# Optimization experiments

Measured on AMD Instinct MI355X. Metric: run time of the kernel, lower is better.

## Reference

```python
import jax, jax.numpy as jnp
import numpy as np

F = 256   # nb_features
H = 8     # nb_heads
B = 4
S = 1024  # q_s == kv_s
SCALE = F ** 0.5  # module MULTIPLIES scores by sqrt(f) when scale=True


def setup_inputs() -> dict:
    key = jax.random.key(0)
    ks = jax.random.split(key, 6)
    return {
        "q_input": jax.random.normal(ks[0], (B, F, S), dtype=jnp.float32),
        "kv_input": jax.random.normal(ks[1], (B, F, S), dtype=jnp.float32),
        "Wq": jax.random.normal(ks[2], (F, F * H), dtype=jnp.float32) * (F ** -0.5),
        "Wk": jax.random.normal(ks[3], (F, F * H), dtype=jnp.float32) * (F ** -0.5),
        "Wv": jax.random.normal(ks[4], (F, F * H), dtype=jnp.float32) * (F ** -0.5),
        "Wz": jax.random.normal(ks[5], (F * H, F), dtype=jnp.float32) * ((F * H) ** -0.5),
    }


def reference(q_input, kv_input, Wq, Wk, Wv, Wz):
    b, f, q_s = q_input.shape
    kv_s = kv_input.shape[2]
    h = H
    # (b, f, s) -> (b, s, f)
    qx = jnp.transpose(q_input, (0, 2, 1))
    kvx = jnp.transpose(kv_input, (0, 2, 1))
    # Linear f -> f*h, then split last dim into (f, h)
    q = (qx @ Wq).reshape(b, q_s, f, h)
    k = (kvx @ Wk).reshape(b, kv_s, f, h)
    v = (kvx @ Wv).reshape(b, kv_s, f, h)
    # sigmoid-gated attention: scores MULTIPLIED by sqrt(f)
    qkt = jnp.einsum('bifh,bjfh->bijh', q, k)
    attn = jax.nn.sigmoid(qkt * SCALE)
    weighted_v = jnp.einsum('bijh,bjfh->bifh', attn, v)  # (b, q_s, f, h)
    z = weighted_v.reshape(b * q_s, f * h)
    out = jax.nn.relu(z @ Wz)  # dropout p=0.0 -> identity
    return jnp.transpose(out.reshape(b, q_s, f), (0, 2, 1))  # (b, f, q_s)
```

## Files before the change

kernel.cpp:

```cpp
#include <hip/hip_runtime.h>
#include <hip/hip_fp16.h>

typedef _Float16 f16;
typedef _Float16 f16x8 __attribute__((ext_vector_type(8)));
typedef float f32x4 __attribute__((ext_vector_type(4)));

#define AS1(p) ((const __attribute__((address_space(1))) void*)(p))
#define AS3(p) ((__attribute__((address_space(3))) void*)(p))

__device__ __forceinline__ void gload16(const void* g, void* l) {
  __builtin_amdgcn_global_load_lds(AS1(g), AS3(l), 16, 0, 0);
}

__device__ __forceinline__ float sgm(float x) {
  return __builtin_amdgcn_rcpf(1.0f + __builtin_amdgcn_exp2f(x * -23.083120654223414f));
}

__device__ __forceinline__ unsigned pack2(float a, float b) {
  union { f16 h[2]; unsigned u; } x;
  x.h[0] = (f16)a; x.h[1] = (f16)b;
  return x.u;
}

__device__ __forceinline__ void tbody(const float* __restrict__ ip,
                                      f16* __restrict__ op,
                                      long in_rs, long out_rs) {
  __shared__ float t[64][68];
  int tid = threadIdx.x;
  {
    int c4 = (tid & 15) * 4, r0 = tid >> 4;
#pragma unroll
    for (int p = 0; p < 4; ++p) {
      int r = r0 + 16 * p;
      float4 v = *(const float4*)(ip + (long)r * in_rs + c4);
      t[c4 + 0][r] = v.x; t[c4 + 1][r] = v.y; t[c4 + 2][r] = v.z; t[c4 + 3][r] = v.w;
    }
  }
  __syncthreads();
  {
    int r4 = (tid & 15) * 4, c0 = tid >> 4;
#pragma unroll
    for (int p = 0; p < 4; ++p) {
      int c = c0 + 16 * p;
      float4 v = *(const float4*)(&t[c][r4]);
      union { f16 h[4]; unsigned long long u; } pk;
      pk.h[0] = (f16)v.x; pk.h[1] = (f16)v.y; pk.h[2] = (f16)v.z; pk.h[3] = (f16)v.w;
      *(unsigned long long*)(op + (long)c * out_rs + r4) = pk.u;
    }
  }
}

__global__ __launch_bounds__(256) void tin(const float* __restrict__ qin,
                                           const float* __restrict__ kvin,
                                           f16* __restrict__ Xq, f16* __restrict__ Xkv) {
  int z = blockIdx.z;
  const float* in = (z < 4) ? qin : kvin;
  f16* out = (z < 4) ? Xq : Xkv;
  long b = z & 3;
  tbody(in + b * 262144 + (long)(blockIdx.y * 64) * 1024 + blockIdx.x * 64,
        out + b * 262144 + (long)(blockIdx.x * 64) * 256 + blockIdx.y * 64,
        1024, 256);
}

__global__ __launch_bounds__(256) void tw3(const float* __restrict__ Wq,
                                           const float* __restrict__ Wk,
                                           const float* __restrict__ Wv,
                                           f16* __restrict__ Wqt, f16* __restrict__ Wkt,
                                           f16* __restrict__ Wvt) {
  int z = blockIdx.z;
  const float* in = (z == 0) ? Wq : (z == 1) ? Wk : Wv;
  f16* out = (z == 0) ? Wqt : (z == 1) ? Wkt : Wvt;
  tbody(in + (long)(blockIdx.y * 64) * 2048 + blockIdx.x * 64,
        out + (long)(blockIdx.x * 64) * 256 + blockIdx.y * 64,
        2048, 256);
}

__global__ __launch_bounds__(256) void twz(const float* __restrict__ Wz,
                                           f16* __restrict__ Wzt) {
  long z = blockIdx.z;
  tbody(Wz + z * 256 + (long)(blockIdx.y * 64) * 2048 + blockIdx.x * 64,
        Wzt + z * 256 + (long)(blockIdx.x * 64) * 2048 + blockIdx.y * 64,
        2048, 2048);
}

__global__ __launch_bounds__(256) void projk(
    const f16* __restrict__ Xq, const f16* __restrict__ Xkv,
    const f16* __restrict__ Wqt, const f16* __restrict__ Wkt, const f16* __restrict__ Wvt,
    f16* __restrict__ Qh, f16* __restrict__ Kh, f16* __restrict__ Vt) {
  __shared__ char sm[65536];
  int z = blockIdx.z;
  const f16* A = (z == 0) ? Xq : Xkv;
  const f16* B = (z == 0) ? Wqt : (z == 1) ? Wkt : Wvt;
  int m0 = blockIdx.x * 128, n0 = blockIdx.y * 128;
  int tid = threadIdx.x, wave = tid >> 6, lane = tid & 63;
  int wm = wave & 1, wn = wave >> 1;
  f32x4 acc[4][4];
#pragma unroll
  for (int i = 0; i < 4; ++i)
#pragma unroll
    for (int j = 0; j < 4; ++j) acc[i][j] = (f32x4){0.f, 0.f, 0.f, 0.f};

  auto PSTAGE = [&](int buf, int kt) {
    char* As = sm + buf * 32768;
    char* Bs = As + 16384;
    int k0 = kt * 64;
#pragma unroll
    for (int is = 0; is < 4; ++is) {
      int loff = is * 4096 + wave * 1024;
      int g = loff + lane * 16;
      int row = g >> 7, sl = (g >> 4) & 7;
      int sp = (sl ^ (row & 7)) * 8;
      gload16(A + (long)(m0 + row) * 256 + k0 + sp, As + loff);
      gload16(B + (long)(n0 + row) * 256 + k0 + sp, Bs + loff);
    }
  };

  PSTAGE(0, 0);
  __syncthreads();
  for (int kt = 0; kt < 4; ++kt) {
    int cur = kt & 1;
    if (kt < 3) PSTAGE(cur ^ 1, kt + 1);
    const char* As = sm + cur * 32768;
    const char* Bs = As + 16384;
#pragma unroll
    for (int t = 0; t < 2; ++t) {
      f16x8 af[4], bf[4];
#pragma unroll
      for (int mi = 0; mi < 4; ++mi) {
        int row = wm * 64 + mi * 16 + (lane & 15);
        int sl = (t * 4 + (lane >> 4)) ^ (row & 7);
        af[mi] = *(const f16x8*)(As + row * 128 + sl * 16);
      }
#pragma unroll
      for (int ni = 0; ni < 4; ++ni) {
        int row = wn * 64 + ni * 16 + (lane & 15);
        int sl = (t * 4 + (lane >> 4)) ^ (row & 7);
        bf[ni] = *(const f16x8*)(Bs + row * 128 + sl * 16);
      }
#pragma unroll
      for (int mi = 0; mi < 4; ++mi)
#pragma unroll
        for (int ni = 0; ni < 4; ++ni)
          acc[mi][ni] = __builtin_amdgcn_mfma_f32_16x16x32_f16(af[mi], bf[ni], acc[mi][ni], 0, 0, 0);
    }
    __syncthreads();
  }
#pragma unroll
  for (int mi = 0; mi < 4; ++mi)
#pragma unroll
    for (int ni = 0; ni < 4; ++ni) {
      int cc = wn * 64 + ni * 16 + (lane & 15);
      int rs0 = wm * 64 + mi * 16 + (lane >> 4) * 4;
      union { f16 h[4]; unsigned long long u; } pk;
#pragma unroll
      for (int r = 0; r < 4; ++r) pk.h[r] = (f16)acc[mi][ni][r];
      *(unsigned long long*)(sm + cc * 272 + rs0 * 2) = pk.u;
    }
  __syncthreads();
  if (z < 2) {
    f16* outp = (z == 0) ? Qh : Kh;
#pragma unroll
    for (int pass = 0; pass < 4; ++pass) {
      int item = pass * 256 + tid;
      int rs = item & 127, h = item >> 7;
      int m = m0 + rs, b = m >> 10, s = m & 1023;
      union { unsigned short u16[16]; uint4 q[2]; } pk;
#pragma unroll
      for (int u = 0; u < 16; ++u)
        pk.u16[u] = *(const unsigned short*)(sm + (h + 8 * u) * 272 + rs * 2);
      f16* dst = outp + ((long)(b * 8 + h) * 1024 + s) * 256 + (n0 >> 3);
      *(uint4*)dst = pk.q[0];
      *(uint4*)(dst + 8) = pk.q[1];
    }
  } else {
    int cc = tid >> 1, half = tid & 1;
    int c = n0 + cc, h = c & 7, fi = c >> 3;
    int m = m0 + half * 64;
    int b = m >> 10, s0 = m & 1023;
    uint4 q[8];
#pragma unroll
    for (int j = 0; j < 8; ++j)
      q[j] = *(const uint4*)(sm + cc * 272 + half * 128 + j * 16);
    f16* dst = Vt + ((long)(b * 8 + h) * 256 + fi) * 1024 + s0;
#pragma unroll
    for (int j = 0; j < 8; ++j) *(uint4*)(dst + j * 8) = q[j];
  }
}

__global__ __launch_bounds__(256) void attnk(
    const f16* __restrict__ Qh, const f16* __restrict__ Kh,
    const f16* __restrict__ Vt, f16* __restrict__ Zb) {
  __shared__ char sm[65536];
  int flat = blockIdx.x;
  int xcd = flat & 7, slotb = flat >> 3;
  int bh = xcd + 8 * (slotb & 3);
  int i0 = (slotb >> 2) * 64;
  int tid = threadIdx.x, wave = tid >> 6, lane = tid & 63;
  int l15 = lane & 15, l4 = lane >> 4;
  const f16* Qp = Qh + (long)bh * 262144;
  const f16* Kp = Kh + (long)bh * 262144;
  const f16* Vp = Vt + (long)bh * 262144;
  f16x8 q[8];
  {
    const f16* qr = Qp + (long)(i0 + wave * 16 + l15) * 256 + l4 * 8;
#pragma unroll
    for (int t = 0; t < 8; ++t) q[t] = *(const f16x8*)(qr + t * 32);
  }
  f32x4 acc[16];
#pragma unroll
  for (int n = 0; n < 16; ++n) acc[n] = (f32x4){0.f, 0.f, 0.f, 0.f};

  auto STAGE = [&](int buf, int j0) {
    char* Ks = sm + buf * 32768;
    char* Vs = Ks + 16384;
#pragma unroll
    for (int is = 0; is < 4; ++is) {
      int loff = is * 4096 + wave * 1024;
      int g = loff + lane * 16;
      {
        int row = g >> 9, sl = (g >> 4) & 31;
        gload16(Kp + (long)(j0 + row) * 256 + ((sl ^ row) * 8), Ks + loff);
      }
      {
        int f = g >> 6, jc = (g >> 4) & 3;
        gload16(Vp + (long)f * 1024 + j0 + jc * 8, Vs + loff);
      }
    }
  };

  STAGE(0, 0);
  __syncthreads();
  for (int jt = 0; jt < 32; ++jt) {
    int cur = jt & 1;
    if (jt < 31) STAGE(cur ^ 1, (jt + 1) * 32);
    const char* Ks = sm + cur * 32768;
    const char* Vs = Ks + 16384;
    f32x4 s0 = (f32x4){0.f, 0.f, 0.f, 0.f};
    f32x4 s1 = (f32x4){0.f, 0.f, 0.f, 0.f};
#pragma unroll
    for (int t = 0; t < 8; ++t) {
      int c = t * 4 + l4;
      f16x8 k0 = *(const f16x8*)(Ks + l15 * 512 + ((c ^ l15) * 16));
      f16x8 k1 = *(const f16x8*)(Ks + (16 + l15) * 512 + ((c ^ (16 + l15)) * 16));
      s0 = __builtin_amdgcn_mfma_f32_16x16x32_f16(k0, q[t], s0, 0, 0, 0);
      s1 = __builtin_amdgcn_mfma_f32_16x16x32_f16(k1, q[t], s1, 0, 0, 0);
    }
    unsigned u00 = pack2(sgm(s0[0]), sgm(s0[1]));
    unsigned u01 = pack2(sgm(s0[2]), sgm(s0[3]));
    unsigned u10 = pack2(sgm(s1[0]), sgm(s1[1]));
    unsigned u11 = pack2(sgm(s1[2]), sgm(s1[3]));
    auto a0 = __builtin_amdgcn_permlane32_swap(u00, u10, false, false);
    auto w02 = __builtin_amdgcn_permlane16_swap(a0[0], a0[1], false, false);
    auto a1 = __builtin_amdgcn_permlane32_swap(u01, u11, false, false);
    auto w13 = __builtin_amdgcn_permlane16_swap(a1[0], a1[1], false, false);
    union { unsigned u[4]; f16x8 v; } pa;
    pa.u[0] = w02[0]; pa.u[1] = w13[0]; pa.u[2] = w02[1]; pa.u[3] = w13[1];
#pragma unroll
    for (int n = 0; n < 16; ++n) {
      f16x8 vb = *(const f16x8*)(Vs + (n * 16 + l15) * 64 + l4 * 16);
      acc[n] = __builtin_amdgcn_mfma_f32_16x16x32_f16(pa.v, vb, acc[n], 0, 0, 0);
    }
    __syncthreads();
  }
#pragma unroll
  for (int nf = 0; nf < 16; ++nf)
#pragma unroll
    for (int r = 0; r < 4; ++r) {
      int il = wave * 16 + l4 * 4 + r;
      int f = nf * 16 + l15;
      *(f16*)(sm + il * 512 + ((f * 2) ^ (((il >> 2) & 3) << 5))) = (f16)acc[nf][r];
    }
  __syncthreads();
  f16* zp = Zb + ((long)bh * 1024 + i0) * 256;
#pragma unroll
  for (int c = 0; c < 8; ++c) {
    int il = c * 8 + (tid >> 5);
    int fb = (tid & 31) * 16;
    uint4 v = *(const uint4*)(sm + il * 512 + (fb ^ (((il >> 2) & 3) << 5)));
    *(uint4*)((char*)zp + il * 512 + fb) = v;
  }
}

__global__ __launch_bounds__(256) void zkern(
    const f16* __restrict__ Wzt, const f16* __restrict__ Zb,
    float* __restrict__ out) {
  __shared__ char sm[32768];
  int fo0 = blockIdx.x * 64, s0 = blockIdx.y * 64, b = blockIdx.z;
  int tid = threadIdx.x, wave = tid >> 6, lane = tid & 63;
  int wm = wave & 1, wn = wave >> 1;
  f32x4 acc[2][2];
#pragma unroll
  for (int i = 0; i < 2; ++i)
#pragma unroll
    for (int j = 0; j < 2; ++j) acc[i][j] = (f32x4){0.f, 0.f, 0.f, 0.f};

  auto ZSTAGE = [&](int buf, int kt) {
    char* As = sm + buf * 16384;
    char* Bs = As + 8192;
    int k0 = kt * 64, h = k0 >> 8, fi0 = k0 & 255;
#pragma unroll
    for (int is = 0; is < 2; ++is) {
      int loff = is * 4096 + wave * 1024;
      int g = loff + lane * 16;
      int row = g >> 7, sl = (g >> 4) & 7;
      int sp = (sl ^ (row & 7)) * 8;
      gload16(Wzt + (long)(fo0 + row) * 2048 + k0 + sp, As + loff);
      gload16(Zb + ((long)(b * 8 + h) * 1024 + s0 + row) * 256 + fi0 + sp, Bs + loff);
    }
  };

  ZSTAGE(0, 0);
  __syncthreads();
  for (int kt = 0; kt < 32; ++kt) {
    int cur = kt & 1;
    if (kt < 31) ZSTAGE(cur ^ 1, kt + 1);
    const char* As = sm + cur * 16384;
    const char* Bs = As + 8192;
#pragma unroll
    for (int t = 0; t < 2; ++t) {
      f16x8 af[2], bf[2];
#pragma unroll
      for (int mi = 0; mi < 2; ++mi) {
        int row = wm * 32 + mi * 16 + (lane & 15);
        int sl = (t * 4 + (lane >> 4)) ^ (row & 7);
        af[mi] = *(const f16x8*)(As + row * 128 + sl * 16);
      }
#pragma unroll
      for (int ni = 0; ni < 2; ++ni) {
        int row = wn * 32 + ni * 16 + (lane & 15);
        int sl = (t * 4 + (lane >> 4)) ^ (row & 7);
        bf[ni] = *(const f16x8*)(Bs + row * 128 + sl * 16);
      }
#pragma unroll
      for (int mi = 0; mi < 2; ++mi)
#pragma unroll
        for (int ni = 0; ni < 2; ++ni)
          acc[mi][ni] = __builtin_amdgcn_mfma_f32_16x16x32_f16(af[mi], bf[ni], acc[mi][ni], 0, 0, 0);
    }
    __syncthreads();
  }
#pragma unroll
  for (int mi = 0; mi < 2; ++mi)
#pragma unroll
    for (int ni = 0; ni < 2; ++ni)
#pragma unroll
      for (int r = 0; r < 4; ++r) {
        int fo = fo0 + wm * 32 + mi * 16 + (lane >> 4) * 4 + r;
        int s = s0 + wn * 32 + ni * 16 + (lane & 15);
        float v = acc[mi][ni][r];
        out[((long)b * 256 + fo) * 1024 + s] = v > 0.f ? v : 0.f;
      }
}

extern "C" void kernel_launch(void* const* d_in, const int* in_sizes, int n_in,
                              void* d_out, int out_size, void* d_ws, size_t ws_size,
                              hipStream_t stream) {
  const float* qin = (const float*)d_in[0];
  const float* kvin = (const float*)d_in[1];
  const float* Wq = (const float*)d_in[2];
  const float* Wk = (const float*)d_in[3];
  const float* Wv = (const float*)d_in[4];
  const float* Wz = (const float*)d_in[5];
  float* out = (float*)d_out;
  char* ws = (char*)d_ws;
  const long MB = 1 << 20;
  f16* Xq  = (f16*)(ws + 0 * MB);
  f16* Xkv = (f16*)(ws + 2 * MB);
  f16* Wqt = (f16*)(ws + 4 * MB);
  f16* Wkt = (f16*)(ws + 5 * MB);
  f16* Wvt = (f16*)(ws + 6 * MB);
  f16* Wzt = (f16*)(ws + 7 * MB);
  f16* Qh  = (f16*)(ws + 8 * MB);
  f16* Kh  = (f16*)(ws + 24 * MB);
  f16* Vt  = (f16*)(ws + 40 * MB);
  f16* Zb  = Qh;
  dim3 blk(256);
  tin<<<dim3(16, 4, 8), blk, 0, stream>>>(qin, kvin, Xq, Xkv);
  tw3<<<dim3(32, 4, 3), blk, 0, stream>>>(Wq, Wk, Wv, Wqt, Wkt, Wvt);
  twz<<<dim3(4, 4, 8), blk, 0, stream>>>(Wz, Wzt);
  projk<<<dim3(32, 16, 3), blk, 0, stream>>>(Xq, Xkv, Wqt, Wkt, Wvt, Qh, Kh, Vt);
  attnk<<<dim3(512), blk, 0, stream>>>(Qh, Kh, Vt, Zb);
  zkern<<<dim3(4, 16, 4), blk, 0, stream>>>(Wzt, Zb, out);
}
```

Measured before the change: 128.1 us.

## Merge transpose kernels and streamline attention loop addressing and scheduling

The three input and weight transpose kernels are merged into one launch over a flat grid of 1024 blocks, removing two kernel launches. In the attention kernel, global K/V pointers are precomputed and advanced each tile instead of recomputing addresses. The V tile in LDS gets an XOR swizzle to reduce bank conflicts, and buffer selection is done by XOR on offsets. The loop also adds s_setprio around the MFMA sections and uses cvt_pkrtz for the fp16 packing, which rounds toward zero instead of to nearest.

Result: faster. 118.2 us (-7.7%).

```diff
diff --git a/kernel.cpp b/kernel.cpp
--- a/kernel.cpp
+++ b/kernel.cpp
@@ -3,7 +3,9 @@
 
 typedef _Float16 f16;
 typedef _Float16 f16x8 __attribute__((ext_vector_type(8)));
+typedef _Float16 h16x2 __attribute__((ext_vector_type(2)));
 typedef float f32x4 __attribute__((ext_vector_type(4)));
+typedef unsigned u32x4 __attribute__((ext_vector_type(4)));
 
 #define AS1(p) ((const __attribute__((address_space(1))) void*)(p))
 #define AS3(p) ((__attribute__((address_space(3))) void*)(p))
@@ -14,12 +16,6 @@
 
 __device__ __forceinline__ float sgm(float x) {
   return __builtin_amdgcn_rcpf(1.0f + __builtin_amdgcn_exp2f(x * -23.083120654223414f));
-}
-
-__device__ __forceinline__ unsigned pack2(float a, float b) {
-  union { f16 h[2]; unsigned u; } x;
-  x.h[0] = (f16)a; x.h[1] = (f16)b;
-  return x.u;
 }
 
 __device__ __forceinline__ void tbody(const float* __restrict__ ip,
@@ -50,37 +46,35 @@
   }
 }
 
-__global__ __launch_bounds__(256) void tin(const float* __restrict__ qin,
-                                           const float* __restrict__ kvin,
-                                           f16* __restrict__ Xq, f16* __restrict__ Xkv) {
-  int z = blockIdx.z;
-  const float* in = (z < 4) ? qin : kvin;
-  f16* out = (z < 4) ? Xq : Xkv;
-  long b = z & 3;
-  tbody(in + b * 262144 + (long)(blockIdx.y * 64) * 1024 + blockIdx.x * 64,
-        out + b * 262144 + (long)(blockIdx.x * 64) * 256 + blockIdx.y * 64,
-        1024, 256);
-}
-
-__global__ __launch_bounds__(256) void tw3(const float* __restrict__ Wq,
-                                           const float* __restrict__ Wk,
-                                           const float* __restrict__ Wv,
-                                           f16* __restrict__ Wqt, f16* __restrict__ Wkt,
-                                           f16* __restrict__ Wvt) {
-  int z = blockIdx.z;
-  const float* in = (z == 0) ? Wq : (z == 1) ? Wk : Wv;
-  f16* out = (z == 0) ? Wqt : (z == 1) ? Wkt : Wvt;
-  tbody(in + (long)(blockIdx.y * 64) * 2048 + blockIdx.x * 64,
-        out + (long)(blockIdx.x * 64) * 256 + blockIdx.y * 64,
-        2048, 256);
-}
-
-__global__ __launch_bounds__(256) void twz(const float* __restrict__ Wz,
-                                           f16* __restrict__ Wzt) {
-  long z = blockIdx.z;
-  tbody(Wz + z * 256 + (long)(blockIdx.y * 64) * 2048 + blockIdx.x * 64,
-        Wzt + z * 256 + (long)(blockIdx.x * 64) * 2048 + blockIdx.y * 64,
-        2048, 2048);
+__global__ __launch_bounds__(256) void tall(
+    const float* __restrict__ qin, const float* __restrict__ kvin,
+    const float* __restrict__ Wq, const float* __restrict__ Wk,
+    const float* __restrict__ Wv, const float* __restrict__ Wz,
+    f16* __restrict__ Xq, f16* __restrict__ Xkv,
+    f16* __restrict__ Wqt, f16* __restrict__ Wkt, f16* __restrict__ Wvt,
+    f16* __restrict__ Wzt) {
+  int id = blockIdx.x;
+  if (id < 512) {
+    int x = id & 15, y = (id >> 4) & 3, z = id >> 6;
+    const float* in = (z < 4) ? qin : kvin;
+    f16* out = (z < 4) ? Xq : Xkv;
+    long b = z & 3;
+    tbody(in + b * 262144 + (long)(y * 64) * 1024 + x * 64,
+          out + b * 262144 + (long)(x * 64) * 256 + y * 64, 1024, 256);
+  } else if (id < 896) {
+    int t = id - 512;
+    int x = t & 31, y = (t >> 5) & 3, z = t >> 7;
+    const float* in = (z == 0) ? Wq : (z == 1) ? Wk : Wv;
+    f16* out = (z == 0) ? Wqt : (z == 1) ? Wkt : Wvt;
+    tbody(in + (long)(y * 64) * 2048 + x * 64,
+          out + (long)(x * 64) * 256 + y * 64, 2048, 256);
+  } else {
+    int t = id - 896;
+    int x = t & 3, y = (t >> 2) & 3;
+    long z = t >> 4;
+    tbody(Wz + z * 256 + (long)(y * 64) * 2048 + x * 64,
+          Wzt + z * 256 + (long)(x * 64) * 2048 + y * 64, 2048, 2048);
+  }
 }
 
 __global__ __launch_bounds__(256) void projk(
@@ -198,8 +192,6 @@
   int tid = threadIdx.x, wave = tid >> 6, lane = tid & 63;
   int l15 = lane & 15, l4 = lane >> 4;
   const f16* Qp = Qh + (long)bh * 262144;
-  const f16* Kp = Kh + (long)bh * 262144;
-  const f16* Vp = Vt + (long)bh * 262144;
   f16x8 q[8];
   {
     const f16* qr = Qp + (long)(i0 + wave * 16 + l15) * 256 + l4 * 8;
@@ -210,57 +202,72 @@
 #pragma unroll
   for (int n = 0; n < 16; ++n) acc[n] = (f32x4){0.f, 0.f, 0.f, 0.f};
 
-  auto STAGE = [&](int buf, int j0) {
-    char* Ks = sm + buf * 32768;
-    char* Vs = Ks + 16384;
+  const char* kp[4];
+  const char* vp[4];
+  {
+    const char* Kb = (const char*)(Kh + (long)bh * 262144);
+    const char* Vb = (const char*)(Vt + (long)bh * 262144);
 #pragma unroll
     for (int is = 0; is < 4; ++is) {
-      int loff = is * 4096 + wave * 1024;
-      int g = loff + lane * 16;
-      {
-        int row = g >> 9, sl = (g >> 4) & 31;
-        gload16(Kp + (long)(j0 + row) * 256 + ((sl ^ row) * 8), Ks + loff);
-      }
-      {
-        int f = g >> 6, jc = (g >> 4) & 3;
-        gload16(Vp + (long)f * 1024 + j0 + jc * 8, Vs + loff);
-      }
+      int g = is * 4096 + wave * 1024 + lane * 16;
+      int krow = g >> 9, ksl = (g >> 4) & 31;
+      kp[is] = Kb + krow * 512 + ((ksl ^ krow) * 16);
+      int f = g >> 6, jc = (g >> 4) & 3;
+      vp[is] = Vb + f * 2048 + ((jc ^ ((f >> 1) & 3)) * 16);
+    }
+  }
+  const int KB  = l15 * 512 + ((l4 * 16) ^ (l15 * 16));
+  const int KB2 = KB + 8448;
+  const int VB  = 16384 + l15 * 64 + ((l4 ^ ((l15 >> 1) & 3)) * 16);
+  const int sdo = wave * 1024;
+
+  auto STAGE = [&](int ob) {
+#pragma unroll
+    for (int is = 0; is < 4; ++is) {
+      gload16(kp[is], sm + ob + is * 4096 + sdo);
+      gload16(vp[is], sm + ob + 16384 + is * 4096 + sdo);
+      kp[is] += 16384;
+      vp[is] += 64;
     }
   };
 
-  STAGE(0, 0);
-  __syncthreads();
+  STAGE(0);
+  __syncthreads();
+  int bb = 0;
   for (int jt = 0; jt < 32; ++jt) {
-    int cur = jt & 1;
-    if (jt < 31) STAGE(cur ^ 1, (jt + 1) * 32);
-    const char* Ks = sm + cur * 32768;
-    const char* Vs = Ks + 16384;
+    if (jt < 31) STAGE(bb ^ 32768);
+    const int kb = KB ^ bb, kb2 = KB2 ^ bb, vb = VB ^ bb;
     f32x4 s0 = (f32x4){0.f, 0.f, 0.f, 0.f};
     f32x4 s1 = (f32x4){0.f, 0.f, 0.f, 0.f};
+    __builtin_amdgcn_s_setprio(1);
 #pragma unroll
     for (int t = 0; t < 8; ++t) {
-      int c = t * 4 + l4;
-      f16x8 k0 = *(const f16x8*)(Ks + l15 * 512 + ((c ^ l15) * 16));
-      f16x8 k1 = *(const f16x8*)(Ks + (16 + l15) * 512 + ((c ^ (16 + l15)) * 16));
+      f16x8 k0 = *(const f16x8*)(sm + (kb ^ (t * 64)));
+      f16x8 k1 = *(const f16x8*)(sm + (kb2 ^ (t * 64)));
       s0 = __builtin_amdgcn_mfma_f32_16x16x32_f16(k0, q[t], s0, 0, 0, 0);
       s1 = __builtin_amdgcn_mfma_f32_16x16x32_f16(k1, q[t], s1, 0, 0, 0);
     }
-    unsigned u00 = pack2(sgm(s0[0]), sgm(s0[1]));
-    unsigned u01 = pack2(sgm(s0[2]), sgm(s0[3]));
-    unsigned u10 = pack2(sgm(s1[0]), sgm(s1[1]));
-    unsigned u11 = pack2(sgm(s1[2]), sgm(s1[3]));
+    __builtin_amdgcn_s_setprio(0);
+    unsigned u00 = __builtin_bit_cast(unsigned, __builtin_amdgcn_cvt_pkrtz(sgm(s0[0]), sgm(s0[1])));
+    unsigned u01 = __builtin_bit_cast(unsigned, __builtin_amdgcn_cvt_pkrtz(sgm(s0[2]), sgm(s0[3])));
+    unsigned u10 = __builtin_bit_cast(unsigned, __builtin_amdgcn_cvt_pkrtz(sgm(s1[0]), sgm(s1[1])));
+    unsigned u11 = __builtin_bit_cast(unsigned, __builtin_amdgcn_cvt_pkrtz(sgm(s1[2]), sgm(s1[3])));
     auto a0 = __builtin_amdgcn_permlane32_swap(u00, u10, false, false);
     auto w02 = __builtin_amdgcn_permlane16_swap(a0[0], a0[1], false, false);
     auto a1 = __builtin_amdgcn_permlane32_swap(u01, u11, false, false);
     auto w13 = __builtin_amdgcn_permlane16_swap(a1[0], a1[1], false, false);
-    union { unsigned u[4]; f16x8 v; } pa;
-    pa.u[0] = w02[0]; pa.u[1] = w13[0]; pa.u[2] = w02[1]; pa.u[3] = w13[1];
+    u32x4 paw;
+    paw[0] = w02[0]; paw[1] = w13[0]; paw[2] = w02[1]; paw[3] = w13[1];
+    f16x8 pav = __builtin_bit_cast(f16x8, paw);
+    __builtin_amdgcn_s_setprio(1);
 #pragma unroll
     for (int n = 0; n < 16; ++n) {
-      f16x8 vb = *(const f16x8*)(Vs + (n * 16 + l15) * 64 + l4 * 16);
-      acc[n] = __builtin_amdgcn_mfma_f32_16x16x32_f16(pa.v, vb, acc[n], 0, 0, 0);
-    }
+      f16x8 vbf = *(const f16x8*)(sm + (vb ^ (n * 1024)));
+      acc[n] = __builtin_amdgcn_mfma_f32_16x16x32_f16(pav, vbf, acc[n], 0, 0, 0);
+    }
+    __builtin_amdgcn_s_setprio(0);
     __syncthreads();
+    bb ^= 32768;
   }
 #pragma unroll
   for (int nf = 0; nf < 16; ++nf)
@@ -375,9 +382,8 @@
   f16* Vt  = (f16*)(ws + 40 * MB);
   f16* Zb  = Qh;
   dim3 blk(256);
-  tin<<<dim3(16, 4, 8), blk, 0, stream>>>(qin, kvin, Xq, Xkv);
-  tw3<<<dim3(32, 4, 3), blk, 0, stream>>>(Wq, Wk, Wv, Wqt, Wkt, Wvt);
-  twz<<<dim3(4, 4, 8), blk, 0, stream>>>(Wz, Wzt);
+  tall<<<dim3(1024), blk, 0, stream>>>(qin, kvin, Wq, Wk, Wv, Wz,
+                                       Xq, Xkv, Wqt, Wkt, Wvt, Wzt);
   projk<<<dim3(32, 16, 3), blk, 0, stream>>>(Xq, Xkv, Wqt, Wkt, Wvt, Qh, Kh, Vt);
   attnk<<<dim3(512), blk, 0, stream>>>(Qh, Kh, Vt, Zb);
   zkern<<<dim3(4, 16, 4), blk, 0, stream>>>(Wzt, Zb, out);
```
